# Optimization experiments

Measured on AMD Instinct MI355X. Metric: run time of the kernel, lower is better.

## Reference

```python
import jax, jax.numpy as jnp
import numpy as np
import itertools

EPS = 1e-6
# Blade ordering for Cl(3,0): (), e1,e2,e3, e12,e13,e23, e123 -> grade of each blade
GRADE = np.array([0, 1, 1, 1, 2, 2, 2, 3])
_SL = [(0, 1), (1, 4), (4, 7), (7, 8)]  # blade slices per grade subspace


def build_cayley():
    """Geometric-product Cayley table for Cl(3,0) (Euclidean metric)."""
    blades = [()] + [c for r in range(1, 4) for c in itertools.combinations(range(3), r)]
    masks = [sum(1 << i for i in b) for b in blades]
    idx = {m: i for i, m in enumerate(masks)}
    C = np.zeros((8, 8, 8), np.float32)
    for i, a in enumerate(masks):
        for j, b in enumerate(masks):
            s, aa = 0, a >> 1
            while aa:
                s += bin(aa & b).count('1')
                aa >>= 1
            C[i, j, idx[a ^ b]] = -1.0 if (s & 1) else 1.0
    return C


def _qs(x):
    """Quadratic form per grade subspace: [..., 8] -> [..., 4] (Euclidean metric)."""
    x2 = x * x
    return jnp.concatenate([x2[..., a:b].sum(-1, keepdims=True) for a, b in _SL], axis=-1)


def _mvlinear(x, w, b=None):
    """Per-subspace multivector linear. x: [B, m, 8], w: [n, m, 4], b: [n] (scalar blade)."""
    out = jnp.einsum('bmi,nmi->bni', x, w[:, :, GRADE])
    if b is not None:
        out = out.at[..., 0].add(b)
    return out


def setup_inputs() -> dict:
    key = jax.random.key(0)
    ks = jax.random.split(key, 12)
    B, Fin, Fout = 131072, 16, 32
    return dict(
        x=jax.random.normal(ks[0], (B, Fin, 8), jnp.float32),
        w1=jax.random.normal(ks[1], (Fout, Fin, 4), jnp.float32) * float(1.0 / np.sqrt(Fin)),
        b1=jax.random.normal(ks[2], (Fout,), jnp.float32) * 0.1,
        a_relu=jax.random.uniform(ks[3], (Fout, 4), jnp.float32) + 0.5,
        b_relu=jax.random.normal(ks[4], (Fout, 4), jnp.float32) * 0.1,
        wl=jax.random.normal(ks[5], (Fout, Fout, 4), jnp.float32) * float(1.0 / np.sqrt(Fout)),
        bl=jax.random.normal(ks[6], (Fout,), jnp.float32) * 0.1,
        wr=jax.random.normal(ks[7], (Fout, Fout, 4), jnp.float32) * float(1.0 / np.sqrt(Fout)),
        a_norm=jax.random.normal(ks[8], (Fout, 4), jnp.float32) * 0.1,
        gp_w=jax.random.normal(ks[9], (Fout, 4, 4, 4), jnp.float32) * 0.5,
        a_ln=jax.random.uniform(ks[10], (Fout,), jnp.float32) + 0.5,
        cayley=jnp.asarray(build_cayley()),
    )


def reference(x, w1, b1, a_relu, b_relu, wl, bl, wr, a_norm, gp_w, a_ln, cayley):
    # --- MVLinear ---
    h = _mvlinear(x, w1, b1)  # [B, C, 8]
    # --- MVReLU: gate each channel by relu(a * invariants + b), invariants broadcast per grade ---
    inv = jnp.concatenate([h[..., :1], _qs(h)[..., 1:]], axis=-1)  # [B, C, 4]
    h = jax.nn.relu(a_relu * inv + b_relu)[..., GRADE] * h
    # --- SteerableGeometricProductLayer ---
    xr = _mvlinear(h, wr)  # linear_right (no bias)
    n = jnp.sqrt(jnp.abs(_qs(xr)))  # grade-wise norms
    n = jax.nn.sigmoid(a_norm) * (n - 1.0) + 1.0  # learned interpolation toward unit norm
    xr = xr / (n[..., GRADE] + EPS)
    # per-channel steerable geometric product weight: cayley * grade-block weight
    W = cayley[None] * gp_w[:, GRADE][:, :, GRADE][:, :, :, GRADE]  # [C, 8, 8, 8]
    h = (_mvlinear(h, wl, bl) + jnp.einsum('bci,cijk,bck->bcj', h, W, xr)) * float(1.0 / np.sqrt(2.0))
    # --- MVLayerNorm: divide by channel-mean multivector norm ---
    nrm = jnp.sqrt(_qs(h).sum(-1, keepdims=True)).mean(axis=1, keepdims=True) + EPS  # [B, 1, 1]
    return a_ln[:, None] * h / nrm
```

## Files before the change

### kernel.cpp

```cpp
#include <hip/hip_runtime.h>
#include <math.h>

#define EPSV 1e-6f

namespace {

constexpr int FIN   = 16;
constexpr int FOUT  = 32;
constexpr int SLOTS = 8;
constexpr int EPT   = 2;
constexpr int ELEMS = SLOTS * EPT;
constexpr int BLK   = 32 * SLOTS;
constexpr int GRID  = 1024;

constexpr int GJ[8][8] = {
  {0,1,2,3,4,5,6,7},
  {1,0,4,5,2,3,7,6},
  {2,4,0,6,1,7,3,5},
  {3,5,6,0,7,1,2,4},
  {4,2,1,7,0,6,5,3},
  {5,3,7,1,6,0,4,2},
  {6,7,3,2,5,4,0,1},
  {7,6,5,4,3,2,1,0},
};
constexpr float SREF[8][8] = {
  { 1, 1, 1, 1, 1, 1, 1, 1},
  { 1, 1, 1, 1, 1, 1, 1, 1},
  { 1,-1, 1, 1,-1,-1, 1,-1},
  { 1,-1,-1, 1, 1,-1,-1, 1},
  {-1, 1,-1,-1, 1, 1,-1, 1},
  {-1, 1, 1,-1,-1, 1, 1,-1},
  {-1,-1, 1,-1, 1,-1, 1, 1},
  {-1,-1, 1,-1, 1,-1, 1, 1},
};
constexpr int GSLOT[8][8] = {
  {0,1,1,1,2,2,2,3},
  {5,4,7,7,6,6,9,8},
  {5,7,4,7,6,9,6,8},
  {5,7,7,4,9,6,6,8},
  {13,11,11,15,10,14,14,12},
  {13,11,15,11,14,10,14,12},
  {13,15,11,11,14,14,10,12},
  {19,18,18,18,17,17,17,16},
};
constexpr int SLOT_OFF[20] = {0,5,10,15,17,20,22,25,27,30,34,37,39,40,42,45,51,54,57,60};

}

__global__ __launch_bounds__(BLK, 3)
void cge_block_kernel(const float* __restrict__ x,
                      const float* __restrict__ w1,
                      const float* __restrict__ b1,
                      const float* __restrict__ a_relu,
                      const float* __restrict__ b_relu,
                      const float* __restrict__ wl,
                      const float* __restrict__ bl,
                      const float* __restrict__ wr,
                      const float* __restrict__ a_norm,
                      const float* __restrict__ gp_w,
                      const float* __restrict__ a_ln,
                      float* __restrict__ out,
                      int B)
{
  __shared__ float4 w1s[FIN * FOUT];
  __shared__ float4 wrs[FOUT * FOUT];
  __shared__ float4 xs[2][ELEMS * FIN];
  __shared__ float4 hs[2][ELEMS * FOUT];

  const int tid  = threadIdx.x;
  const int c    = tid & 31;
  const int slot = tid >> 5;

  for (int idx = tid; idx < FIN * FOUT; idx += BLK) {
    int cc = idx >> 4, m = idx & 15;
    w1s[m * FOUT + cc] = ((const float4*)w1)[idx];
  }
  for (int idx = tid; idx < FOUT * FOUT; idx += BLK) {
    int cc = idx >> 5, m = idx & 31;
    wrs[m * FOUT + cc] = ((const float4*)wr)[idx];
  }

  float gw[20];
#pragma unroll
  for (int s = 0; s < 20; ++s) gw[s] = gp_w[c * 64 + SLOT_OFF[s]];
  const float  b1c  = b1[c];
  const float  blc  = bl[c];
  const float  alnc = a_ln[c];
  const float4 ar   = ((const float4*)a_relu)[c];
  const float4 br   = ((const float4*)b_relu)[c];
  const float4 an   = ((const float4*)a_norm)[c];
  const float  sg0  = 1.f / (1.f + expf(-an.x));
  const float  sg1  = 1.f / (1.f + expf(-an.y));
  const float  sg2  = 1.f / (1.f + expf(-an.z));
  const float  sg3  = 1.f / (1.f + expf(-an.w));
  const float4* wlc = ((const float4*)wl) + c * FOUT;

  const int ngroups = B / ELEMS;

  for (int g = blockIdx.x; g < ngroups; g += gridDim.x) {
    const int eb = g * ELEMS;
    __syncthreads();

    {
      const float4* xg = ((const float4*)x) + (size_t)eb * (FIN * 2);
#pragma unroll
      for (int t = 0; t < (ELEMS * FIN * 2) / BLK; ++t) {
        int idx = tid + t * BLK;
        float4 v = xg[idx];
        int e = idx >> 5, r = idx & 31;
        xs[r & 1][e * FIN + (r >> 1)] = v;
      }
    }
    __syncthreads();

    float h0[EPT][8];
#pragma unroll
    for (int e = 0; e < EPT; ++e) {
      h0[e][0] = b1c;
#pragma unroll
      for (int i = 1; i < 8; ++i) h0[e][i] = 0.f;
    }
#pragma unroll 4
    for (int m = 0; m < FIN; ++m) {
      const float4 w = w1s[m * FOUT + c];
#pragma unroll
      for (int e = 0; e < EPT; ++e) {
        const int le = slot * EPT + e;
        const float4 xlo = xs[0][le * FIN + m];
        const float4 xhi = xs[1][le * FIN + m];
        h0[e][0] += xlo.x * w.x;
        h0[e][1] += xlo.y * w.y;
        h0[e][2] += xlo.z * w.y;
        h0[e][3] += xlo.w * w.y;
        h0[e][4] += xhi.x * w.z;
        h0[e][5] += xhi.y * w.z;
        h0[e][6] += xhi.z * w.z;
        h0[e][7] += xhi.w * w.w;
      }
    }
#pragma unroll
    for (int e = 0; e < EPT; ++e) {
      const int le = slot * EPT + e;
      const float q1 = h0[e][1]*h0[e][1] + h0[e][2]*h0[e][2] + h0[e][3]*h0[e][3];
      const float q2 = h0[e][4]*h0[e][4] + h0[e][5]*h0[e][5] + h0[e][6]*h0[e][6];
      const float q3 = h0[e][7]*h0[e][7];
      const float g0 = fmaxf(ar.x * h0[e][0] + br.x, 0.f);
      const float g1 = fmaxf(ar.y * q1 + br.y, 0.f);
      const float g2 = fmaxf(ar.z * q2 + br.z, 0.f);
      const float g3 = fmaxf(ar.w * q3 + br.w, 0.f);
      h0[e][0] *= g0;
      h0[e][1] *= g1; h0[e][2] *= g1; h0[e][3] *= g1;
      h0[e][4] *= g2; h0[e][5] *= g2; h0[e][6] *= g2;
      h0[e][7] *= g3;
      hs[0][le * FOUT + c] = make_float4(h0[e][0], h0[e][1], h0[e][2], h0[e][3]);
      hs[1][le * FOUT + c] = make_float4(h0[e][4], h0[e][5], h0[e][6], h0[e][7]);
    }
    __syncthreads();

    float xr[EPT][8];
#pragma unroll
    for (int e = 0; e < EPT; ++e)
#pragma unroll
      for (int i = 0; i < 8; ++i) xr[e][i] = 0.f;
#pragma unroll 4
    for (int m = 0; m < FOUT; ++m) {
      const float4 w = wrs[m * FOUT + c];
#pragma unroll
      for (int e = 0; e < EPT; ++e) {
        const int le = slot * EPT + e;
        const float4 hlo = hs[0][le * FOUT + m];
        const float4 hhi = hs[1][le * FOUT + m];
        xr[e][0] += hlo.x * w.x;
        xr[e][1] += hlo.y * w.y;
        xr[e][2] += hlo.z * w.y;
        xr[e][3] += hlo.w * w.y;
        xr[e][4] += hhi.x * w.z;
        xr[e][5] += hhi.y * w.z;
        xr[e][6] += hhi.z * w.z;
        xr[e][7] += hhi.w * w.w;
      }
    }
#pragma unroll
    for (int e = 0; e < EPT; ++e) {
      const float q0 = xr[e][0]*xr[e][0];
      const float q1 = xr[e][1]*xr[e][1] + xr[e][2]*xr[e][2] + xr[e][3]*xr[e][3];
      const float q2 = xr[e][4]*xr[e][4] + xr[e][5]*xr[e][5] + xr[e][6]*xr[e][6];
      const float q3 = xr[e][7]*xr[e][7];
      const float r0 = 1.f / (sg0 * (sqrtf(q0) - 1.f) + 1.f + EPSV);
      const float r1 = 1.f / (sg1 * (sqrtf(q1) - 1.f) + 1.f + EPSV);
      const float r2 = 1.f / (sg2 * (sqrtf(q2) - 1.f) + 1.f + EPSV);
      const float r3 = 1.f / (sg3 * (sqrtf(q3) - 1.f) + 1.f + EPSV);
      xr[e][0] *= r0;
      xr[e][1] *= r1; xr[e][2] *= r1; xr[e][3] *= r1;
      xr[e][4] *= r2; xr[e][5] *= r2; xr[e][6] *= r2;
      xr[e][7] *= r3;
    }

    float h2[EPT][8];
#pragma unroll
    for (int e = 0; e < EPT; ++e) {
      h2[e][0] = blc;
#pragma unroll
      for (int i = 1; i < 8; ++i) h2[e][i] = 0.f;
    }
#pragma unroll 4
    for (int m = 0; m < FOUT; ++m) {
      const float4 w = wlc[m];
#pragma unroll
      for (int e = 0; e < EPT; ++e) {
        const int le = slot * EPT + e;
        const float4 hlo = hs[0][le * FOUT + m];
        const float4 hhi = hs[1][le * FOUT + m];
        h2[e][0] += hlo.x * w.x;
        h2[e][1] += hlo.y * w.y;
        h2[e][2] += hlo.z * w.y;
        h2[e][3] += hlo.w * w.y;
        h2[e][4] += hhi.x * w.z;
        h2[e][5] += hhi.y * w.z;
        h2[e][6] += hhi.z * w.z;
        h2[e][7] += hhi.w * w.w;
      }
    }
#pragma unroll
    for (int i = 0; i < 8; ++i) {
#pragma unroll
      for (int k = 0; k < 8; ++k) {
        const float w = SREF[i][k] * gw[GSLOT[i][k]];
#pragma unroll
        for (int e = 0; e < EPT; ++e) {
          h2[e][GJ[i][k]] += (w * h0[e][i]) * xr[e][k];
        }
      }
    }

#pragma unroll
    for (int e = 0; e < EPT; ++e) {
      const int le = slot * EPT + e;
      float s = 0.f;
#pragma unroll
      for (int i = 0; i < 8; ++i) {
        h2[e][i] *= 0.70710678118654752f;
        s += h2[e][i] * h2[e][i];
      }
      float n = sqrtf(s);
      n += __shfl_xor(n, 1);
      n += __shfl_xor(n, 2);
      n += __shfl_xor(n, 4);
      n += __shfl_xor(n, 8);
      n += __shfl_xor(n, 16);
      const float scale = alnc / (n * (1.f / FOUT) + EPSV);
      float4* o4 = (float4*)out + (size_t)(eb + le) * (FOUT * 2) + c * 2;
      o4[0] = make_float4(h2[e][0] * scale, h2[e][1] * scale,
                          h2[e][2] * scale, h2[e][3] * scale);
      o4[1] = make_float4(h2[e][4] * scale, h2[e][5] * scale,
                          h2[e][6] * scale, h2[e][7] * scale);
    }
  }
}

extern "C" void kernel_launch(void* const* d_in, const int* in_sizes, int n_in,
                              void* d_out, int out_size, void* d_ws, size_t ws_size,
                              hipStream_t stream) {
  const float* x      = (const float*)d_in[0];
  const float* w1     = (const float*)d_in[1];
  const float* b1     = (const float*)d_in[2];
  const float* a_relu = (const float*)d_in[3];
  const float* b_relu = (const float*)d_in[4];
  const float* wl     = (const float*)d_in[5];
  const float* bl     = (const float*)d_in[6];
  const float* wr     = (const float*)d_in[7];
  const float* a_norm = (const float*)d_in[8];
  const float* gp_w   = (const float*)d_in[9];
  const float* a_ln   = (const float*)d_in[10];

  const int B = in_sizes[0] / (FIN * 8);
  const int ngroups = B / ELEMS;
  const int grid = ngroups < GRID ? ngroups : GRID;

  cge_block_kernel<<<grid, BLK, 0, stream>>>(
      x, w1, b1, a_relu, b_relu, wl, bl, wr, a_norm, gp_w, a_ln,
      (float*)d_out, B);
}
```

Baseline: 406.5 us.

## Read x directly from global, fuse wr/wl matmuls, raise occupancy hint

Result: slower. 435.0 us (+7.0%).

```diff
diff --git a/kernel.cpp b/kernel.cpp
--- a/kernel.cpp
+++ b/kernel.cpp
@@ -7,10 +7,9 @@
 
 constexpr int FIN   = 16;
 constexpr int FOUT  = 32;
-constexpr int SLOTS = 8;
 constexpr int EPT   = 2;
-constexpr int ELEMS = SLOTS * EPT;
-constexpr int BLK   = 32 * SLOTS;
+constexpr int ELEMS = 8 * EPT;
+constexpr int BLK   = 256;
 constexpr int GRID  = 1024;
 
 constexpr int GJ[8][8] = {
@@ -47,7 +46,7 @@
 
 }
 
-__global__ __launch_bounds__(BLK, 3)
+__global__ __launch_bounds__(BLK, 4)
 void cge_block_kernel(const float* __restrict__ x,
                       const float* __restrict__ w1,
                       const float* __restrict__ b1,
@@ -64,7 +63,6 @@
 {
   __shared__ float4 w1s[FIN * FOUT];
   __shared__ float4 wrs[FOUT * FOUT];
-  __shared__ float4 xs[2][ELEMS * FIN];
   __shared__ float4 hs[2][ELEMS * FOUT];
 
   const int tid  = threadIdx.x;
@@ -94,24 +92,14 @@
   const float  sg2  = 1.f / (1.f + expf(-an.z));
   const float  sg3  = 1.f / (1.f + expf(-an.w));
   const float4* wlc = ((const float4*)wl) + c * FOUT;
+  const float4* xg  = (const float4*)x;
+
+  __syncthreads();
 
   const int ngroups = B / ELEMS;
 
   for (int g = blockIdx.x; g < ngroups; g += gridDim.x) {
     const int eb = g * ELEMS;
-    __syncthreads();
-
-    {
-      const float4* xg = ((const float4*)x) + (size_t)eb * (FIN * 2);
-#pragma unroll
-      for (int t = 0; t < (ELEMS * FIN * 2) / BLK; ++t) {
-        int idx = tid + t * BLK;
-        float4 v = xg[idx];
-        int e = idx >> 5, r = idx & 31;
-        xs[r & 1][e * FIN + (r >> 1)] = v;
-      }
-    }
-    __syncthreads();
 
     float h0[EPT][8];
 #pragma unroll
@@ -126,8 +114,9 @@
 #pragma unroll
       for (int e = 0; e < EPT; ++e) {
         const int le = slot * EPT + e;
-        const float4 xlo = xs[0][le * FIN + m];
-        const float4 xhi = xs[1][le * FIN + m];
+        const size_t xb = (size_t)(eb + le) * (FIN * 2) + 2 * m;
+        const float4 xlo = xg[xb];
+        const float4 xhi = xg[xb + 1];
         h0[e][0] += xlo.x * w.x;
         h0[e][1] += xlo.y * w.y;
         h0[e][2] += xlo.z * w.y;
@@ -140,7 +129,6 @@
     }
 #pragma unroll
     for (int e = 0; e < EPT; ++e) {
-      const int le = slot * EPT + e;
       const float q1 = h0[e][1]*h0[e][1] + h0[e][2]*h0[e][2] + h0[e][3]*h0[e][3];
       const float q2 = h0[e][4]*h0[e][4] + h0[e][5]*h0[e][5] + h0[e][6]*h0[e][6];
       const float q3 = h0[e][7]*h0[e][7];
@@ -152,34 +140,45 @@
       h0[e][1] *= g1; h0[e][2] *= g1; h0[e][3] *= g1;
       h0[e][4] *= g2; h0[e][5] *= g2; h0[e][6] *= g2;
       h0[e][7] *= g3;
+    }
+
+    __syncthreads();
+#pragma unroll
+    for (int e = 0; e < EPT; ++e) {
+      const int le = slot * EPT + e;
       hs[0][le * FOUT + c] = make_float4(h0[e][0], h0[e][1], h0[e][2], h0[e][3]);
       hs[1][le * FOUT + c] = make_float4(h0[e][4], h0[e][5], h0[e][6], h0[e][7]);
     }
     __syncthreads();
 
-    float xr[EPT][8];
-#pragma unroll
-    for (int e = 0; e < EPT; ++e)
-#pragma unroll
-      for (int i = 0; i < 8; ++i) xr[e][i] = 0.f;
-#pragma unroll 4
+    float xr[EPT][8], hl[EPT][8];
+#pragma unroll
+    for (int e = 0; e < EPT; ++e) {
+      hl[e][0] = blc;
+      xr[e][0] = 0.f;
+#pragma unroll
+      for (int i = 1; i < 8; ++i) { xr[e][i] = 0.f; hl[e][i] = 0.f; }
+    }
+#pragma unroll 2
     for (int m = 0; m < FOUT; ++m) {
-      const float4 w = wrs[m * FOUT + c];
+      const float4 wrv = wrs[m * FOUT + c];
+      const float4 wlv = wlc[m];
 #pragma unroll
       for (int e = 0; e < EPT; ++e) {
         const int le = slot * EPT + e;
         const float4 hlo = hs[0][le * FOUT + m];
         const float4 hhi = hs[1][le * FOUT + m];
-        xr[e][0] += hlo.x * w.x;
-        xr[e][1] += hlo.y * w.y;
-        xr[e][2] += hlo.z * w.y;
-        xr[e][3] += hlo.w * w.y;
-        xr[e][4] += hhi.x * w.z;
-        xr[e][5] += hhi.y * w.z;
-        xr[e][6] += hhi.z * w.z;
-        xr[e][7] += hhi.w * w.w;
-      }
-    }
+        xr[e][0] += hlo.x * wrv.x;  hl[e][0] += hlo.x * wlv.x;
+        xr[e][1] += hlo.y * wrv.y;  hl[e][1] += hlo.y * wlv.y;
+        xr[e][2] += hlo.z * wrv.y;  hl[e][2] += hlo.z * wlv.y;
+        xr[e][3] += hlo.w * wrv.y;  hl[e][3] += hlo.w * wlv.y;
+        xr[e][4] += hhi.x * wrv.z;  hl[e][4] += hhi.x * wlv.z;
+        xr[e][5] += hhi.y * wrv.z;  hl[e][5] += hhi.y * wlv.z;
+        xr[e][6] += hhi.z * wrv.z;  hl[e][6] += hhi.z * wlv.z;
+        xr[e][7] += hhi.w * wrv.w;  hl[e][7] += hhi.w * wlv.w;
+      }
+    }
+
 #pragma unroll
     for (int e = 0; e < EPT; ++e) {
       const float q0 = xr[e][0]*xr[e][0];
@@ -196,31 +195,6 @@
       xr[e][7] *= r3;
     }
 
-    float h2[EPT][8];
-#pragma unroll
-    for (int e = 0; e < EPT; ++e) {
-      h2[e][0] = blc;
-#pragma unroll
-      for (int i = 1; i < 8; ++i) h2[e][i] = 0.f;
-    }
-#pragma unroll 4
-    for (int m = 0; m < FOUT; ++m) {
-      const float4 w = wlc[m];
-#pragma unroll
-      for (int e = 0; e < EPT; ++e) {
-        const int le = slot * EPT + e;
-        const float4 hlo = hs[0][le * FOUT + m];
-        const float4 hhi = hs[1][le * FOUT + m];
-        h2[e][0] += hlo.x * w.x;
-        h2[e][1] += hlo.y * w.y;
-        h2[e][2] += hlo.z * w.y;
-        h2[e][3] += hlo.w * w.y;
-        h2[e][4] += hhi.x * w.z;
-        h2[e][5] += hhi.y * w.z;
-        h2[e][6] += hhi.z * w.z;
-        h2[e][7] += hhi.w * w.w;
-      }
-    }
 #pragma unroll
     for (int i = 0; i < 8; ++i) {
 #pragma unroll
@@ -228,7 +202,7 @@
         const float w = SREF[i][k] * gw[GSLOT[i][k]];
 #pragma unroll
         for (int e = 0; e < EPT; ++e) {
-          h2[e][GJ[i][k]] += (w * h0[e][i]) * xr[e][k];
+          hl[e][GJ[i][k]] += (w * h0[e][i]) * xr[e][k];
         }
       }
     }
@@ -239,8 +213,8 @@
       float s = 0.f;
 #pragma unroll
       for (int i = 0; i < 8; ++i) {
-        h2[e][i] *= 0.70710678118654752f;
-        s += h2[e][i] * h2[e][i];
+        hl[e][i] *= 0.70710678118654752f;
+        s += hl[e][i] * hl[e][i];
       }
       float n = sqrtf(s);
       n += __shfl_xor(n, 1);
@@ -250,10 +224,10 @@
       n += __shfl_xor(n, 16);
       const float scale = alnc / (n * (1.f / FOUT) + EPSV);
       float4* o4 = (float4*)out + (size_t)(eb + le) * (FOUT * 2) + c * 2;
-      o4[0] = make_float4(h2[e][0] * scale, h2[e][1] * scale,
-                          h2[e][2] * scale, h2[e][3] * scale);
-      o4[1] = make_float4(h2[e][4] * scale, h2[e][5] * scale,
-                          h2[e][6] * scale, h2[e][7] * scale);
+      o4[0] = make_float4(hl[e][0] * scale, hl[e][1] * scale,
+                          hl[e][2] * scale, hl[e][3] * scale);
+      o4[1] = make_float4(hl[e][4] * scale, hl[e][5] * scale,
+                          hl[e][6] * scale, hl[e][7] * scale);
     }
   }
 }
```
